# Performance work log

Hardware: AMD Instinct MI355X
Metric: run time of the kernel (lower is better)

## Reference

```python
import jax, jax.numpy as jnp
import numpy as np

NEAR, FAR = 0.0, 6.0
N_COARSE, N_IMP = 128, 64
W = 256


def _sdf_net(p, params):
    w0, b0, w1, b1, w2, b2, w3, b3 = params
    h = jax.nn.softplus(p @ w0 + b0)
    h = jax.nn.softplus(h @ w1 + b1)
    h = jax.nn.softplus(h @ w2 + b2)
    out = h @ w3 + b3  # [..., 1 + W]
    return out[..., 0], out[..., 1:]


def _laplace_cdf(x, beta):
    # CDF of zero-mean Laplace with scale beta (VolSDF density)
    return jnp.where(x <= 0, 0.5 * jnp.exp(x / beta), 1.0 - 0.5 * jnp.exp(-x / beta))


def _sample_pdf(bins, weights, n_samples):
    # bins [R, Nc], weights [R, Nc-1] -> [R, n_samples] (deterministic, perturb=False)
    w = weights + 1e-5
    pdf = w / jnp.sum(w, -1, keepdims=True)
    cdf = jnp.concatenate([jnp.zeros_like(pdf[..., :1]), jnp.cumsum(pdf, -1)], -1)  # [R, Nc]
    u = jnp.linspace(0.0, 1.0, n_samples, dtype=bins.dtype)
    u = jnp.broadcast_to(u, (*bins.shape[:-1], n_samples))
    inds = jax.vmap(jnp.searchsorted)(cdf, u)
    below = jnp.clip(inds - 1, 0, cdf.shape[-1] - 1)
    above = jnp.clip(inds, 0, cdf.shape[-1] - 1)
    cdf_b = jnp.take_along_axis(cdf, below, -1)
    cdf_a = jnp.take_along_axis(cdf, above, -1)
    bin_b = jnp.take_along_axis(bins, below, -1)
    bin_a = jnp.take_along_axis(bins, above, -1)
    denom = jnp.where(cdf_a - cdf_b < 1e-5, 1.0, cdf_a - cdf_b)
    t = (u - cdf_b) / denom
    return bin_b + t * (bin_a - bin_b)


def _transmittance_weights(sigma, deltas):
    a = 1.0 - jnp.exp(-sigma * deltas)
    T = jnp.cumprod(jnp.concatenate([jnp.ones_like(a[..., :1]), 1.0 - a + 1e-10], -1), -1)[..., :-1]
    return a * T


def _render(rays_o, rays_d, alpha, beta, sdf_params, rad_params):
    rays_d = rays_d / jnp.linalg.norm(rays_d, axis=-1, keepdims=True)
    R = rays_o.shape[0]
    a_net = alpha[0]
    b_net = beta[0]
    t = jnp.linspace(0.0, 1.0, N_COARSE, dtype=rays_o.dtype)
    d_coarse = jnp.broadcast_to(NEAR * (1.0 - t) + FAR * t, (R, N_COARSE))

    # --- hierarchical fine sampling (torch.no_grad() in source -> stop_gradient) ---
    pts_c = rays_o[:, None, :] + rays_d[:, None, :] * d_coarse[..., None]
    sdf_c, _ = _sdf_net(pts_c, sdf_params)
    sigma_c = a_net * _laplace_cdf(-sdf_c, b_net)
    deltas_c = jnp.diff(d_coarse, axis=-1)
    w_c = _transmittance_weights(sigma_c[..., :-1], deltas_c)
    d_fine = jax.lax.stop_gradient(_sample_pdf(d_coarse, w_c, N_IMP))

    d_all = jnp.sort(jnp.concatenate([d_coarse, d_fine], -1), -1)  # [R, Nc+Nf]
    pts = rays_o[:, None, :] + rays_d[:, None, :] * d_all[..., None]

    sdf, feat = _sdf_net(pts, sdf_params)
    # analytic surface normals: nabla_p sdf(p)
    grad_fn = jax.grad(lambda p: _sdf_net(p, sdf_params)[0])
    nablas = jax.vmap(grad_fn)(pts.reshape(-1, 3)).reshape(pts.shape)
    normals = nablas / (jnp.linalg.norm(nablas, axis=-1, keepdims=True) + 1e-7)

    vdirs = jnp.broadcast_to(rays_d[:, None, :], pts.shape)
    w0, b0, w1, b1, w2, b2 = rad_params
    h = jnp.concatenate([pts, vdirs, normals, feat], -1)  # [R, Nt, 265]
    h = jax.nn.relu(h @ w0 + b0)
    h = jax.nn.relu(h @ w1 + b1)
    rgb = jax.nn.sigmoid(h @ w2 + b2)  # [R, Nt, 3]

    sigma = a_net * _laplace_cdf(-sdf, b_net)
    deltas = jnp.concatenate([jnp.diff(d_all, axis=-1), jnp.full_like(d_all[..., :1], 1e10)], -1)
    weights = _transmittance_weights(sigma, deltas)  # [R, Nt]
    rgb_map = jnp.sum(weights[..., None] * rgb, axis=-2)  # [R, 3]
    return rgb_map


def setup_inputs() -> dict:
    key = jax.random.key(0)
    ks = jax.random.split(key, 16)
    R = 2048

    def w(k, shape):
        return (jax.random.normal(k, shape, dtype=jnp.float32) / np.sqrt(shape[0])).astype(jnp.float32)

    return {
        'rays_o': jax.random.normal(ks[0], (R, 3), dtype=jnp.float32),
        'rays_d': jax.random.normal(ks[1], (R, 3), dtype=jnp.float32),
        'alpha': jnp.ones((1,), dtype=jnp.float32),
        'beta': jnp.ones((1,), dtype=jnp.float32),
        'sdf_w0': w(ks[2], (3, W)), 'sdf_b0': jnp.zeros((W,), jnp.float32),
        'sdf_w1': w(ks[3], (W, W)), 'sdf_b1': jnp.zeros((W,), jnp.float32),
        'sdf_w2': w(ks[4], (W, W)), 'sdf_b2': jnp.zeros((W,), jnp.float32),
        'sdf_w3': w(ks[5], (W, W + 1)), 'sdf_b3': jnp.zeros((W + 1,), jnp.float32),
        'rad_w0': w(ks[6], (9 + W, W)), 'rad_b0': jnp.zeros((W,), jnp.float32),
        'rad_w1': w(ks[7], (W, W)), 'rad_b1': jnp.zeros((W,), jnp.float32),
        'rad_w2': w(ks[8], (W, 3)), 'rad_b2': jnp.zeros((3,), jnp.float32),
    }


def reference(rays_o, rays_d, alpha, beta,
              sdf_w0, sdf_b0, sdf_w1, sdf_b1, sdf_w2, sdf_b2, sdf_w3, sdf_b3,
              rad_w0, rad_b0, rad_w1, rad_b1, rad_w2, rad_b2):
    sdf_params = (sdf_w0, sdf_b0, sdf_w1, sdf_b1, sdf_w2, sdf_b2, sdf_w3, sdf_b3)
    rad_params = (rad_w0, rad_b0, rad_w1, rad_b1, rad_w2, rad_b2)
    return _render(rays_o, rays_d, alpha, beta, sdf_params, rad_params)
```

## Files before the change

### kernel.cpp

```cpp
#include <hip/hip_runtime.h>
#include <math.h>

#define RAYS 2048

__device__ __forceinline__ float sp_act(float x) {
    return fmaxf(x, 0.0f) + log1pf(expf(-fabsf(x)));
}
__device__ __forceinline__ float lap_cdf(float x, float beta) {
    return (x <= 0.0f) ? 0.5f * expf(x / beta) : 1.0f - 0.5f * expf(-x / beta);
}
__device__ __forceinline__ float sigm(float x) { return 1.0f / (1.0f + expf(-x)); }

template<int MODE, bool BIAS>
__device__ __forceinline__ void tile_mm(const float* __restrict__ Wm,
                                        const float* __restrict__ bias,
                                        const float* IN, float* OUT)
{
    const int t  = threadIdx.x;
    const int j0 = (t & 63) << 2;
    const int p0 = (t >> 6) << 2;
    float acc[4][4];
#pragma unroll
    for (int a = 0; a < 4; ++a)
#pragma unroll
        for (int b = 0; b < 4; ++b) acc[a][b] = 0.0f;

    for (int k = 0; k < 256; k += 4) {
        const float4 w0 = *(const float4*)(Wm + (k + 0) * 256 + j0);
        const float4 w1 = *(const float4*)(Wm + (k + 1) * 256 + j0);
        const float4 w2 = *(const float4*)(Wm + (k + 2) * 256 + j0);
        const float4 w3 = *(const float4*)(Wm + (k + 3) * 256 + j0);
#pragma unroll
        for (int pp = 0; pp < 4; ++pp) {
            const float4 av = *(const float4*)(IN + (p0 + pp) * 256 + k);
            acc[pp][0] = fmaf(av.x, w0.x, acc[pp][0]);
            acc[pp][1] = fmaf(av.x, w0.y, acc[pp][1]);
            acc[pp][2] = fmaf(av.x, w0.z, acc[pp][2]);
            acc[pp][3] = fmaf(av.x, w0.w, acc[pp][3]);
            acc[pp][0] = fmaf(av.y, w1.x, acc[pp][0]);
            acc[pp][1] = fmaf(av.y, w1.y, acc[pp][1]);
            acc[pp][2] = fmaf(av.y, w1.z, acc[pp][2]);
            acc[pp][3] = fmaf(av.y, w1.w, acc[pp][3]);
            acc[pp][0] = fmaf(av.z, w2.x, acc[pp][0]);
            acc[pp][1] = fmaf(av.z, w2.y, acc[pp][1]);
            acc[pp][2] = fmaf(av.z, w2.z, acc[pp][2]);
            acc[pp][3] = fmaf(av.z, w2.w, acc[pp][3]);
            acc[pp][0] = fmaf(av.w, w3.x, acc[pp][0]);
            acc[pp][1] = fmaf(av.w, w3.y, acc[pp][1]);
            acc[pp][2] = fmaf(av.w, w3.z, acc[pp][2]);
            acc[pp][3] = fmaf(av.w, w3.w, acc[pp][3]);
        }
    }
    float bv0 = 0.f, bv1 = 0.f, bv2 = 0.f, bv3 = 0.f;
    if constexpr (BIAS) { bv0 = bias[j0]; bv1 = bias[j0+1]; bv2 = bias[j0+2]; bv3 = bias[j0+3]; }
#pragma unroll
    for (int pp = 0; pp < 4; ++pp) {
        float r0 = acc[pp][0] + bv0;
        float r1 = acc[pp][1] + bv1;
        float r2 = acc[pp][2] + bv2;
        float r3 = acc[pp][3] + bv3;
        if constexpr (MODE == 1) { r0 = sp_act(r0); r1 = sp_act(r1); r2 = sp_act(r2); r3 = sp_act(r3); }
        if constexpr (MODE == 2) { r0 = fmaxf(r0,0.f); r1 = fmaxf(r1,0.f); r2 = fmaxf(r2,0.f); r3 = fmaxf(r3,0.f); }
        *(float4*)(OUT + (p0 + pp) * 256 + j0) = make_float4(r0, r1, r2, r3);
    }
}

__device__ __forceinline__ void rad0_mm(const float* __restrict__ Wm,
                                        const float* __restrict__ bias,
                                        const float (*in9)[12],
                                        const float* F, float* OUT)
{
    const int t  = threadIdx.x;
    const int j0 = (t & 63) << 2;
    const int p0 = (t >> 6) << 2;
    float acc[4][4];
#pragma unroll
    for (int a = 0; a < 4; ++a)
#pragma unroll
        for (int b = 0; b < 4; ++b) acc[a][b] = 0.0f;

#pragma unroll
    for (int k = 0; k < 9; ++k) {
        const float4 w = *(const float4*)(Wm + k * 256 + j0);
#pragma unroll
        for (int pp = 0; pp < 4; ++pp) {
            const float a = in9[p0 + pp][k];
            acc[pp][0] = fmaf(a, w.x, acc[pp][0]);
            acc[pp][1] = fmaf(a, w.y, acc[pp][1]);
            acc[pp][2] = fmaf(a, w.z, acc[pp][2]);
            acc[pp][3] = fmaf(a, w.w, acc[pp][3]);
        }
    }
    for (int k = 0; k < 256; k += 4) {
        const float4 w0 = *(const float4*)(Wm + (9 + k + 0) * 256 + j0);
        const float4 w1 = *(const float4*)(Wm + (9 + k + 1) * 256 + j0);
        const float4 w2 = *(const float4*)(Wm + (9 + k + 2) * 256 + j0);
        const float4 w3 = *(const float4*)(Wm + (9 + k + 3) * 256 + j0);
#pragma unroll
        for (int pp = 0; pp < 4; ++pp) {
            const float4 av = *(const float4*)(F + (p0 + pp) * 256 + k);
            acc[pp][0] = fmaf(av.x, w0.x, acc[pp][0]);
            acc[pp][1] = fmaf(av.x, w0.y, acc[pp][1]);
            acc[pp][2] = fmaf(av.x, w0.z, acc[pp][2]);
            acc[pp][3] = fmaf(av.x, w0.w, acc[pp][3]);
            acc[pp][0] = fmaf(av.y, w1.x, acc[pp][0]);
            acc[pp][1] = fmaf(av.y, w1.y, acc[pp][1]);
            acc[pp][2] = fmaf(av.y, w1.z, acc[pp][2]);
            acc[pp][3] = fmaf(av.y, w1.w, acc[pp][3]);
            acc[pp][0] = fmaf(av.z, w2.x, acc[pp][0]);
            acc[pp][1] = fmaf(av.z, w2.y, acc[pp][1]);
            acc[pp][2] = fmaf(av.z, w2.z, acc[pp][2]);
            acc[pp][3] = fmaf(av.z, w2.w, acc[pp][3]);
            acc[pp][0] = fmaf(av.w, w3.x, acc[pp][0]);
            acc[pp][1] = fmaf(av.w, w3.y, acc[pp][1]);
            acc[pp][2] = fmaf(av.w, w3.z, acc[pp][2]);
            acc[pp][3] = fmaf(av.w, w3.w, acc[pp][3]);
        }
    }
#pragma unroll
    for (int pp = 0; pp < 4; ++pp) {
        float r0 = fmaxf(acc[pp][0] + bias[j0+0], 0.f);
        float r1 = fmaxf(acc[pp][1] + bias[j0+1], 0.f);
        float r2 = fmaxf(acc[pp][2] + bias[j0+2], 0.f);
        float r3 = fmaxf(acc[pp][3] + bias[j0+3], 0.f);
        *(float4*)(OUT + (p0 + pp) * 256 + j0) = make_float4(r0, r1, r2, r3);
    }
}

__global__ __launch_bounds__(256) void prep_kernel(
    const float* __restrict__ w1, const float* __restrict__ w2, const float* __restrict__ w3,
    float* __restrict__ w1T, float* __restrict__ w2T,
    float* __restrict__ w3f, float* __restrict__ w3c0)
{
    const int idx = blockIdx.x * 256 + threadIdx.x;
    const int r = idx >> 8, c = idx & 255;
    w1T[idx] = w1[c * 256 + r];
    w2T[idx] = w2[c * 256 + r];
    w3f[idx] = w3[r * 257 + 1 + c];
    if (idx < 256) w3c0[idx] = w3[idx * 257];
}

__global__ __launch_bounds__(256) void coarse_kernel(
    const float* __restrict__ rays_o, const float* __restrict__ rays_d,
    const float* __restrict__ w0, const float* __restrict__ b0,
    const float* __restrict__ w1, const float* __restrict__ b1,
    const float* __restrict__ w2, const float* __restrict__ b2,
    const float* __restrict__ w3c0, const float* __restrict__ b3,
    float* __restrict__ sdf_out)
{
    __shared__ float A[16 * 256];
    __shared__ float B[16 * 256];
    __shared__ float pts[16][3];
    const int t = threadIdx.x;
    const int base = blockIdx.x * 16;

    if (t < 16) {
        int pg = base + t;
        int ray = pg >> 7, i = pg & 127;
        float ox = rays_o[ray*3+0], oy = rays_o[ray*3+1], oz = rays_o[ray*3+2];
        float dx = rays_d[ray*3+0], dy = rays_d[ray*3+1], dz = rays_d[ray*3+2];
        float n = sqrtf(dx*dx + dy*dy + dz*dz);
        dx /= n; dy /= n; dz /= n;
        float dv = 6.0f * ((float)i / 127.0f);
        pts[t][0] = ox + dx * dv; pts[t][1] = oy + dy * dv; pts[t][2] = oz + dz * dv;
    }
    __syncthreads();
    {
        float wa = w0[t], wb = w0[256 + t], wc = w0[512 + t], bb = b0[t];
#pragma unroll
        for (int p = 0; p < 16; ++p) {
            float z = fmaf(pts[p][0], wa, fmaf(pts[p][1], wb, fmaf(pts[p][2], wc, bb)));
            A[p * 256 + t] = sp_act(z);
        }
    }
    __syncthreads();
    tile_mm<1, true>(w1, b1, A, B); __syncthreads();
    tile_mm<1, true>(w2, b2, B, A); __syncthreads();
    if (t < 16) {
        float s = b3[0];
        for (int k = 0; k < 256; ++k) s = fmaf(A[t * 256 + k], w3c0[k], s);
        sdf_out[base + t] = s;
    }
}

__global__ __launch_bounds__(256) void sample_kernel(
    const float* __restrict__ sdf_c,
    const float* __restrict__ alpha_p, const float* __restrict__ beta_p,
    float* __restrict__ d_all_g)
{
    __shared__ float sig[4][128];
    __shared__ float dc[4][128];
    __shared__ float wbuf[4][127];
    __shared__ float cdf[4][128];
    __shared__ float dfine[4][64];
    __shared__ float dall[4][192];
    const int t = threadIdx.x;
    const int wv = t >> 6, lane = t & 63;
    const int ray = blockIdx.x * 4 + wv;
    const float alpha = alpha_p[0], beta = beta_p[0];

    for (int i = lane; i < 128; i += 64) {
        float s = sdf_c[ray * 128 + i];
        sig[wv][i] = alpha * lap_cdf(-s, beta);
        dc[wv][i] = 6.0f * ((float)i / 127.0f);
    }
    __syncthreads();
    if (lane == 0) {
        float T = 1.0f, S = 0.0f;
        for (int i = 0; i < 127; ++i) {
            float delta = dc[wv][i + 1] - dc[wv][i];
            float a = 1.0f - expf(-sig[wv][i] * delta);
            float w = a * T;
            T *= (1.0f - a + 1e-10f);
            wbuf[wv][i] = w;
            S += (w + 1e-5f);
        }
        float c = 0.0f;
        cdf[wv][0] = 0.0f;
        for (int i = 0; i < 127; ++i) {
            c += (wbuf[wv][i] + 1e-5f) / S;
            cdf[wv][i + 1] = c;
        }
    }
    __syncthreads();
    {
        float u = (float)lane / 63.0f;
        int lo = 0, hi = 128;
        while (lo < hi) { int m = (lo + hi) >> 1; if (cdf[wv][m] < u) lo = m + 1; else hi = m; }
        int below = lo - 1; if (below < 0) below = 0; if (below > 127) below = 127;
        int above = lo; if (above > 127) above = 127;
        float cb = cdf[wv][below], ca = cdf[wv][above];
        float bb = dc[wv][below], ba = dc[wv][above];
        float den = ca - cb; if (den < 1e-5f) den = 1.0f;
        float tt = (u - cb) / den;
        dfine[wv][lane] = bb + tt * (ba - bb);
    }
    __syncthreads();
    {
        float v = dfine[wv][lane];
        int lo = 0, hi = 128;
        while (lo < hi) { int m = (lo + hi) >> 1; if (dc[wv][m] <= v) lo = m + 1; else hi = m; }
        dall[wv][lane + lo] = v;
    }
    for (int i = lane; i < 128; i += 64) {
        float v = dc[wv][i];
        int lo = 0, hi = 64;
        while (lo < hi) { int m = (lo + hi) >> 1; if (dfine[wv][m] < v) lo = m + 1; else hi = m; }
        dall[wv][i + lo] = v;
    }
    __syncthreads();
    for (int i = lane; i < 192; i += 64) d_all_g[ray * 192 + i] = dall[wv][i];
}

__global__ __launch_bounds__(256) void fine_kernel(
    const float* __restrict__ rays_o, const float* __restrict__ rays_d,
    const float* __restrict__ dall_g,
    const float* __restrict__ w0, const float* __restrict__ b0,
    const float* __restrict__ w1, const float* __restrict__ b1,
    const float* __restrict__ w2, const float* __restrict__ b2,
    const float* __restrict__ w3f, const float* __restrict__ w3c0,
    const float* __restrict__ b3,
    const float* __restrict__ w1T, const float* __restrict__ w2T,
    const float* __restrict__ rw0, const float* __restrict__ rb0,
    const float* __restrict__ rw1, const float* __restrict__ rb1,
    const float* __restrict__ rw2, const float* __restrict__ rb2,
    float* __restrict__ fsdf, float* __restrict__ frgb)
{
    __shared__ float X[16 * 256];
    __shared__ float Y[16 * 256];
    __shared__ float Z[16 * 256];
    __shared__ float F[16 * 256];
    __shared__ float in9[16][12];
    const int t = threadIdx.x;
    const int base = blockIdx.x * 16;

    if (t < 16) {
        int pg = base + t;
        int ray = pg / 192, i = pg - ray * 192;
        float ox = rays_o[ray*3+0], oy = rays_o[ray*3+1], oz = rays_o[ray*3+2];
        float dx = rays_d[ray*3+0], dy = rays_d[ray*3+1], dz = rays_d[ray*3+2];
        float n = sqrtf(dx*dx + dy*dy + dz*dz);
        dx /= n; dy /= n; dz /= n;
        float dv = dall_g[ray * 192 + i];
        in9[t][0] = ox + dx * dv; in9[t][1] = oy + dy * dv; in9[t][2] = oz + dz * dv;
        in9[t][3] = dx; in9[t][4] = dy; in9[t][5] = dz;
    }
    __syncthreads();
    {
        float wa = w0[t], wb = w0[256 + t], wc = w0[512 + t], bb = b0[t];
#pragma unroll
        for (int p = 0; p < 16; ++p) {
            float z = fmaf(in9[p][0], wa, fmaf(in9[p][1], wb, fmaf(in9[p][2], wc, bb)));
            X[p * 256 + t] = sp_act(z);
        }
    }
    __syncthreads();
    tile_mm<1, true>(w1, b1, X, Y); __syncthreads();
    tile_mm<1, true>(w2, b2, Y, X); __syncthreads();
    tile_mm<0, true>(w3f, b3 + 1, X, F); __syncthreads();
    if (t < 16) {
        float s = b3[0];
        for (int k = 0; k < 256; ++k) s = fmaf(X[t * 256 + k], w3c0[k], s);
        fsdf[base + t] = s;
    }
    __syncthreads();
    {
        float wc0 = w3c0[t];
#pragma unroll
        for (int p = 0; p < 16; ++p) {
            float h = X[p * 256 + t];
            X[p * 256 + t] = (1.0f - expf(-h)) * wc0;
        }
    }
    __syncthreads();
    tile_mm<0, false>(w2T, nullptr, X, Z); __syncthreads();
    {
#pragma unroll
        for (int p = 0; p < 16; ++p) {
            float h = Y[p * 256 + t];
            Z[p * 256 + t] *= (1.0f - expf(-h));
        }
    }
    __syncthreads();
    tile_mm<0, false>(w1T, nullptr, Z, X); __syncthreads();
    {
        float wa = w0[t], wb = w0[256 + t], wc = w0[512 + t], bb = b0[t];
#pragma unroll
        for (int p = 0; p < 16; ++p) {
            float z = fmaf(in9[p][0], wa, fmaf(in9[p][1], wb, fmaf(in9[p][2], wc, bb)));
            X[p * 256 + t] *= sigm(z);
        }
    }
    __syncthreads();
    if (t < 48) {
        int p = t / 3, c = t - p * 3;
        float s = 0.0f;
        for (int k = 0; k < 256; ++k) s = fmaf(w0[c * 256 + k], X[p * 256 + k], s);
        in9[p][6 + c] = s;
    }
    __syncthreads();
    if (t < 16) {
        float nx = in9[t][6], ny = in9[t][7], nz = in9[t][8];
        float inv = 1.0f / (sqrtf(nx*nx + ny*ny + nz*nz) + 1e-7f);
        in9[t][6] = nx * inv; in9[t][7] = ny * inv; in9[t][8] = nz * inv;
    }
    __syncthreads();
    rad0_mm(rw0, rb0, in9, F, Y); __syncthreads();
    tile_mm<2, true>(rw1, rb1, Y, X); __syncthreads();
    if (t < 48) {
        int p = t / 3, c = t - p * 3;
        float s = rb2[c];
        for (int k = 0; k < 256; ++k) s = fmaf(X[p * 256 + k], rw2[k * 3 + c], s);
        frgb[(base + p) * 3 + c] = sigm(s);
    }
}

__global__ __launch_bounds__(256) void composite_kernel(
    const float* __restrict__ dall_g, const float* __restrict__ fsdf,
    const float* __restrict__ frgb,
    const float* __restrict__ alpha_p, const float* __restrict__ beta_p,
    float* __restrict__ out)
{
    __shared__ float aa[4][192];
    __shared__ float da[4][192];
    const int t = threadIdx.x;
    const int wv = t >> 6, lane = t & 63;
    const int ray = blockIdx.x * 4 + wv;
    const float alpha = alpha_p[0], beta = beta_p[0];

    for (int i = lane; i < 192; i += 64) da[wv][i] = dall_g[ray * 192 + i];
    __syncthreads();
    for (int i = lane; i < 192; i += 64) {
        float s = fsdf[ray * 192 + i];
        float sg = alpha * lap_cdf(-s, beta);
        float delta = (i < 191) ? (da[wv][i + 1] - da[wv][i]) : 1e10f;
        aa[wv][i] = 1.0f - expf(-sg * delta);
    }
    __syncthreads();
    if (lane == 0) {
        float T = 1.0f, r0 = 0.f, r1 = 0.f, r2 = 0.f;
        for (int i = 0; i < 192; ++i) {
            float a = aa[wv][i];
            float w = a * T;
            T *= (1.0f - a + 1e-10f);
            const float* rp = frgb + (ray * 192 + i) * 3;
            r0 = fmaf(w, rp[0], r0);
            r1 = fmaf(w, rp[1], r1);
            r2 = fmaf(w, rp[2], r2);
        }
        out[ray * 3 + 0] = r0; out[ray * 3 + 1] = r1; out[ray * 3 + 2] = r2;
    }
}

extern "C" void kernel_launch(void* const* d_in, const int* in_sizes, int n_in,
                              void* d_out, int out_size, void* d_ws, size_t ws_size,
                              hipStream_t stream) {
    const float* rays_o = (const float*)d_in[0];
    const float* rays_d = (const float*)d_in[1];
    const float* alpha  = (const float*)d_in[2];
    const float* beta   = (const float*)d_in[3];
    const float* sw0 = (const float*)d_in[4];
    const float* sb0 = (const float*)d_in[5];
    const float* sw1 = (const float*)d_in[6];
    const float* sb1 = (const float*)d_in[7];
    const float* sw2 = (const float*)d_in[8];
    const float* sb2 = (const float*)d_in[9];
    const float* sw3 = (const float*)d_in[10];
    const float* sb3 = (const float*)d_in[11];
    const float* rw0 = (const float*)d_in[12];
    const float* rb0 = (const float*)d_in[13];
    const float* rw1 = (const float*)d_in[14];
    const float* rb1 = (const float*)d_in[15];
    const float* rw2 = (const float*)d_in[16];
    const float* rb2 = (const float*)d_in[17];

    float* ws = (float*)d_ws;
    float* w1T   = ws;  ws += 65536;
    float* w2T   = ws;  ws += 65536;
    float* w3f   = ws;  ws += 65536;
    float* w3c0  = ws;  ws += 256;
    float* sdf_c = ws;  ws += RAYS * 128;
    float* dall  = ws;  ws += RAYS * 192;
    float* fsdf  = ws;  ws += RAYS * 192;
    float* frgb  = ws;  ws += RAYS * 192 * 3;

    prep_kernel<<<256, 256, 0, stream>>>(sw1, sw2, sw3, w1T, w2T, w3f, w3c0);
    coarse_kernel<<<RAYS * 128 / 16, 256, 0, stream>>>(
        rays_o, rays_d, sw0, sb0, sw1, sb1, sw2, sb2, w3c0, sb3, sdf_c);
    sample_kernel<<<RAYS / 4, 256, 0, stream>>>(sdf_c, alpha, beta, dall);
    fine_kernel<<<RAYS * 192 / 16, 256, 0, stream>>>(
        rays_o, rays_d, dall,
        sw0, sb0, sw1, sb1, sw2, sb2, w3f, w3c0, sb3,
        w1T, w2T, rw0, rb0, rw1, rb1, rw2, rb2,
        fsdf, frgb);
    composite_kernel<<<RAYS / 4, 256, 0, stream>>>(dall, fsdf, frgb, alpha, beta, (float*)d_out);
}
```

Before: 7.496 ms.

## Replace scalar FP32 MLP GEMMs with split-bf16 MFMA matrix-core GEMMs

```diff
diff --git a/kernel.cpp b/kernel.cpp
--- a/kernel.cpp
+++ b/kernel.cpp
@@ -3,6 +3,10 @@
 
 #define RAYS 2048
 
+typedef unsigned short ushort_t;
+typedef short bf16x8 __attribute__((ext_vector_type(8)));
+typedef float f32x4 __attribute__((ext_vector_type(4)));
+
 __device__ __forceinline__ float sp_act(float x) {
     return fmaxf(x, 0.0f) + log1pf(expf(-fabsf(x)));
 }
@@ -11,174 +15,180 @@
 }
 __device__ __forceinline__ float sigm(float x) { return 1.0f / (1.0f + expf(-x)); }
 
-template<int MODE, bool BIAS>
-__device__ __forceinline__ void tile_mm(const float* __restrict__ Wm,
-                                        const float* __restrict__ bias,
-                                        const float* IN, float* OUT)
+__device__ __forceinline__ ushort_t f2bf(float x) {
+    union { float f; unsigned int u; } c; c.f = x;
+    unsigned int u = c.u + 0x7FFF + ((c.u >> 16) & 1);
+    return (ushort_t)(u >> 16);
+}
+__device__ __forceinline__ float bf2f(ushort_t s) {
+    union { unsigned int u; float f; } c; c.u = ((unsigned int)s) << 16;
+    return c.f;
+}
+__device__ __forceinline__ void split2(float v, ushort_t& hi, ushort_t& lo) {
+    hi = f2bf(v);
+    lo = f2bf(v - bf2f(hi));
+}
+template<int P>
+__device__ __forceinline__ int aidx(int p, int n) { return ((n >> 3) * P + p) * 16 + (n & 7); }
+
+__device__ __forceinline__ void mfma16x16x32(f32x4& c, bf16x8 a, bf16x8 b) {
+    asm("v_mfma_f32_16x16x32_bf16 %0, %1, %2, %0" : "+v"(c) : "v"(a), "v"(b));
+}
+
+template<int MODE, int KSTEPS, bool BIAS, int PM, bool SPLIT>
+__device__ __forceinline__ void mfma_gemm(const ushort_t* __restrict__ A,
+                                          const ushort_t* __restrict__ Bp,
+                                          const float* __restrict__ bias,
+                                          ushort_t* __restrict__ OUT)
 {
-    const int t  = threadIdx.x;
-    const int j0 = (t & 63) << 2;
-    const int p0 = (t >> 6) << 2;
-    float acc[4][4];
-#pragma unroll
-    for (int a = 0; a < 4; ++a)
-#pragma unroll
-        for (int b = 0; b < 4; ++b) acc[a][b] = 0.0f;
-
-    for (int k = 0; k < 256; k += 4) {
-        const float4 w0 = *(const float4*)(Wm + (k + 0) * 256 + j0);
-        const float4 w1 = *(const float4*)(Wm + (k + 1) * 256 + j0);
-        const float4 w2 = *(const float4*)(Wm + (k + 2) * 256 + j0);
-        const float4 w3 = *(const float4*)(Wm + (k + 3) * 256 + j0);
-#pragma unroll
-        for (int pp = 0; pp < 4; ++pp) {
-            const float4 av = *(const float4*)(IN + (p0 + pp) * 256 + k);
-            acc[pp][0] = fmaf(av.x, w0.x, acc[pp][0]);
-            acc[pp][1] = fmaf(av.x, w0.y, acc[pp][1]);
-            acc[pp][2] = fmaf(av.x, w0.z, acc[pp][2]);
-            acc[pp][3] = fmaf(av.x, w0.w, acc[pp][3]);
-            acc[pp][0] = fmaf(av.y, w1.x, acc[pp][0]);
-            acc[pp][1] = fmaf(av.y, w1.y, acc[pp][1]);
-            acc[pp][2] = fmaf(av.y, w1.z, acc[pp][2]);
-            acc[pp][3] = fmaf(av.y, w1.w, acc[pp][3]);
-            acc[pp][0] = fmaf(av.z, w2.x, acc[pp][0]);
-            acc[pp][1] = fmaf(av.z, w2.y, acc[pp][1]);
-            acc[pp][2] = fmaf(av.z, w2.z, acc[pp][2]);
-            acc[pp][3] = fmaf(av.z, w2.w, acc[pp][3]);
-            acc[pp][0] = fmaf(av.w, w3.x, acc[pp][0]);
-            acc[pp][1] = fmaf(av.w, w3.y, acc[pp][1]);
-            acc[pp][2] = fmaf(av.w, w3.z, acc[pp][2]);
-            acc[pp][3] = fmaf(av.w, w3.w, acc[pp][3]);
-        }
-    }
-    float bv0 = 0.f, bv1 = 0.f, bv2 = 0.f, bv3 = 0.f;
-    if constexpr (BIAS) { bv0 = bias[j0]; bv1 = bias[j0+1]; bv2 = bias[j0+2]; bv3 = bias[j0+3]; }
-#pragma unroll
-    for (int pp = 0; pp < 4; ++pp) {
-        float r0 = acc[pp][0] + bv0;
-        float r1 = acc[pp][1] + bv1;
-        float r2 = acc[pp][2] + bv2;
-        float r3 = acc[pp][3] + bv3;
-        if constexpr (MODE == 1) { r0 = sp_act(r0); r1 = sp_act(r1); r2 = sp_act(r2); r3 = sp_act(r3); }
-        if constexpr (MODE == 2) { r0 = fmaxf(r0,0.f); r1 = fmaxf(r1,0.f); r2 = fmaxf(r2,0.f); r3 = fmaxf(r3,0.f); }
-        *(float4*)(OUT + (p0 + pp) * 256 + j0) = make_float4(r0, r1, r2, r3);
-    }
-}
-
-__device__ __forceinline__ void rad0_mm(const float* __restrict__ Wm,
-                                        const float* __restrict__ bias,
-                                        const float (*in9)[12],
-                                        const float* F, float* OUT)
-{
-    const int t  = threadIdx.x;
-    const int j0 = (t & 63) << 2;
-    const int p0 = (t >> 6) << 2;
-    float acc[4][4];
-#pragma unroll
-    for (int a = 0; a < 4; ++a)
-#pragma unroll
-        for (int b = 0; b < 4; ++b) acc[a][b] = 0.0f;
-
-#pragma unroll
-    for (int k = 0; k < 9; ++k) {
-        const float4 w = *(const float4*)(Wm + k * 256 + j0);
-#pragma unroll
-        for (int pp = 0; pp < 4; ++pp) {
-            const float a = in9[p0 + pp][k];
-            acc[pp][0] = fmaf(a, w.x, acc[pp][0]);
-            acc[pp][1] = fmaf(a, w.y, acc[pp][1]);
-            acc[pp][2] = fmaf(a, w.z, acc[pp][2]);
-            acc[pp][3] = fmaf(a, w.w, acc[pp][3]);
-        }
-    }
-    for (int k = 0; k < 256; k += 4) {
-        const float4 w0 = *(const float4*)(Wm + (9 + k + 0) * 256 + j0);
-        const float4 w1 = *(const float4*)(Wm + (9 + k + 1) * 256 + j0);
-        const float4 w2 = *(const float4*)(Wm + (9 + k + 2) * 256 + j0);
-        const float4 w3 = *(const float4*)(Wm + (9 + k + 3) * 256 + j0);
-#pragma unroll
-        for (int pp = 0; pp < 4; ++pp) {
-            const float4 av = *(const float4*)(F + (p0 + pp) * 256 + k);
-            acc[pp][0] = fmaf(av.x, w0.x, acc[pp][0]);
-            acc[pp][1] = fmaf(av.x, w0.y, acc[pp][1]);
-            acc[pp][2] = fmaf(av.x, w0.z, acc[pp][2]);
-            acc[pp][3] = fmaf(av.x, w0.w, acc[pp][3]);
-            acc[pp][0] = fmaf(av.y, w1.x, acc[pp][0]);
-            acc[pp][1] = fmaf(av.y, w1.y, acc[pp][1]);
-            acc[pp][2] = fmaf(av.y, w1.z, acc[pp][2]);
-            acc[pp][3] = fmaf(av.y, w1.w, acc[pp][3]);
-            acc[pp][0] = fmaf(av.z, w2.x, acc[pp][0]);
-            acc[pp][1] = fmaf(av.z, w2.y, acc[pp][1]);
-            acc[pp][2] = fmaf(av.z, w2.z, acc[pp][2]);
-            acc[pp][3] = fmaf(av.z, w2.w, acc[pp][3]);
-            acc[pp][0] = fmaf(av.w, w3.x, acc[pp][0]);
-            acc[pp][1] = fmaf(av.w, w3.y, acc[pp][1]);
-            acc[pp][2] = fmaf(av.w, w3.z, acc[pp][2]);
-            acc[pp][3] = fmaf(av.w, w3.w, acc[pp][3]);
-        }
-    }
-#pragma unroll
-    for (int pp = 0; pp < 4; ++pp) {
-        float r0 = fmaxf(acc[pp][0] + bias[j0+0], 0.f);
-        float r1 = fmaxf(acc[pp][1] + bias[j0+1], 0.f);
-        float r2 = fmaxf(acc[pp][2] + bias[j0+2], 0.f);
-        float r3 = fmaxf(acc[pp][3] + bias[j0+3], 0.f);
-        *(float4*)(OUT + (p0 + pp) * 256 + j0) = make_float4(r0, r1, r2, r3);
+    constexpr int P = PM * 16;
+    const int t = threadIdx.x;
+    const int wave = t >> 6, lane = t & 63;
+    const int r16 = lane & 15, kg = lane >> 4;
+    f32x4 acc[PM][4];
+#pragma unroll
+    for (int m = 0; m < PM; ++m)
+#pragma unroll
+        for (int nf = 0; nf < 4; ++nf) acc[m][nf] = 0.0f;
+
+#pragma unroll
+    for (int ks = 0; ks < KSTEPS; ++ks) {
+        bf16x8 ah[PM], al[PM], bh[4], bl[4];
+#pragma unroll
+        for (int m = 0; m < PM; ++m) {
+            const int ab = ((ks * 4 + kg) * P + m * 16 + r16) * 16;
+            ah[m] = *(const bf16x8*)(A + ab);
+            if (SPLIT) al[m] = *(const bf16x8*)(A + ab + 8);
+        }
+#pragma unroll
+        for (int nf = 0; nf < 4; ++nf) {
+            const int n = wave * 64 + nf * 16 + r16;
+            if (SPLIT) {
+                const int bb = ((ks * 256 + n) * 4 + kg) * 16;
+                bh[nf] = *(const bf16x8*)(Bp + bb);
+                bl[nf] = *(const bf16x8*)(Bp + bb + 8);
+            } else {
+                const int bb = ((ks * 256 + n) * 4 + kg) * 8;
+                bh[nf] = *(const bf16x8*)(Bp + bb);
+            }
+        }
+#pragma unroll
+        for (int m = 0; m < PM; ++m)
+#pragma unroll
+            for (int nf = 0; nf < 4; ++nf) {
+                mfma16x16x32(acc[m][nf], ah[m], bh[nf]);
+                if (SPLIT) {
+                    mfma16x16x32(acc[m][nf], ah[m], bl[nf]);
+                    mfma16x16x32(acc[m][nf], al[m], bh[nf]);
+                }
+            }
+    }
+#pragma unroll
+    for (int nf = 0; nf < 4; ++nf) {
+        const int n = wave * 64 + nf * 16 + r16;
+        float bv = 0.0f;
+        if (BIAS) bv = bias[n];
+#pragma unroll
+        for (int m = 0; m < PM; ++m) {
+#pragma unroll
+            for (int r = 0; r < 4; ++r) {
+                const int p = m * 16 + kg * 4 + r;
+                float v = acc[m][nf][r] + bv;
+                if (MODE == 1) v = sp_act(v);
+                if (MODE == 2) v = fmaxf(v, 0.0f);
+                ushort_t hi, lo;
+                split2(v, hi, lo);
+                const int ob = aidx<P>(p, n);
+                OUT[ob] = hi; OUT[ob + 8] = lo;
+            }
+        }
     }
 }
 
 __global__ __launch_bounds__(256) void prep_kernel(
     const float* __restrict__ w1, const float* __restrict__ w2, const float* __restrict__ w3,
-    float* __restrict__ w1T, float* __restrict__ w2T,
-    float* __restrict__ w3f, float* __restrict__ w3c0)
+    const float* __restrict__ rw0, const float* __restrict__ rw1,
+    ushort_t* __restrict__ pw1T, ushort_t* __restrict__ pw2T, ushort_t* __restrict__ pw3T,
+    ushort_t* __restrict__ pw2B, ushort_t* __restrict__ pw1B,
+    ushort_t* __restrict__ pwR1, ushort_t* __restrict__ pwR0,
+    float* __restrict__ w3c0)
 {
-    const int idx = blockIdx.x * 256 + threadIdx.x;
-    const int r = idx >> 8, c = idx & 255;
-    w1T[idx] = w1[c * 256 + r];
-    w2T[idx] = w2[c * 256 + r];
-    w3f[idx] = w3[r * 257 + 1 + c];
-    if (idx < 256) w3c0[idx] = w3[idx * 257];
-}
-
-__global__ __launch_bounds__(256) void coarse_kernel(
+    const int k = blockIdx.x, mat = blockIdx.y, n = threadIdx.x;
+    const int K = (mat == 6) ? 288 : 256;
+    if (k >= K) return;
+    float v = 0.0f; ushort_t* dst = pw1T; bool lite = false;
+    switch (mat) {
+        case 0: v = w1[k * 256 + n]; dst = pw1T; break;
+        case 1: v = w2[k * 256 + n]; dst = pw2T; break;
+        case 2: v = w3[k * 257 + 1 + n]; dst = pw3T;
+                if (n == 0) w3c0[k] = w3[k * 257];
+                break;
+        case 3: v = w2[n * 256 + k]; dst = pw2B; lite = true; break;
+        case 4: v = w1[n * 256 + k]; dst = pw1B; lite = true; break;
+        case 5: v = rw1[k * 256 + n]; dst = pwR1; break;
+        case 6: v = (k < 256) ? rw0[(9 + k) * 256 + n]
+                  : (k < 265 ? rw0[(k - 256) * 256 + n] : 0.0f);
+                dst = pwR0; break;
+    }
+    if (lite) {
+        dst[(((k >> 5) * 256 + n) * 4 + ((k >> 3) & 3)) * 8 + (k & 7)] = f2bf(v);
+    } else {
+        const int b = (((k >> 5) * 256 + n) * 4 + ((k >> 3) & 3)) * 16 + (k & 7);
+        ushort_t hi, lo; split2(v, hi, lo);
+        dst[b] = hi; dst[b + 8] = lo;
+    }
+}
+
+__global__ __launch_bounds__(256, 1) void coarse_kernel(
     const float* __restrict__ rays_o, const float* __restrict__ rays_d,
     const float* __restrict__ w0, const float* __restrict__ b0,
-    const float* __restrict__ w1, const float* __restrict__ b1,
-    const float* __restrict__ w2, const float* __restrict__ b2,
+    const float* __restrict__ b1, const float* __restrict__ b2,
+    const ushort_t* __restrict__ pw1T, const ushort_t* __restrict__ pw2T,
     const float* __restrict__ w3c0, const float* __restrict__ b3,
     float* __restrict__ sdf_out)
 {
-    __shared__ float A[16 * 256];
-    __shared__ float B[16 * 256];
-    __shared__ float pts[16][3];
+    __shared__ ushort_t bufA[32768], bufB[32768];
+    __shared__ float geo[64][3];
+    __shared__ float red[256];
     const int t = threadIdx.x;
-    const int base = blockIdx.x * 16;
-
-    if (t < 16) {
-        int pg = base + t;
-        int ray = pg >> 7, i = pg & 127;
+    const int base = blockIdx.x * 64;
+
+    if (t < 64) {
+        const int p = t, pg = base + p;
+        const int ray = pg >> 7, i = pg & 127;
         float ox = rays_o[ray*3+0], oy = rays_o[ray*3+1], oz = rays_o[ray*3+2];
         float dx = rays_d[ray*3+0], dy = rays_d[ray*3+1], dz = rays_d[ray*3+2];
-        float n = sqrtf(dx*dx + dy*dy + dz*dz);
-        dx /= n; dy /= n; dz /= n;
+        float nm = sqrtf(dx*dx + dy*dy + dz*dz);
+        dx /= nm; dy /= nm; dz /= nm;
         float dv = 6.0f * ((float)i / 127.0f);
-        pts[t][0] = ox + dx * dv; pts[t][1] = oy + dy * dv; pts[t][2] = oz + dz * dv;
-    }
-    __syncthreads();
-    {
-        float wa = w0[t], wb = w0[256 + t], wc = w0[512 + t], bb = b0[t];
-#pragma unroll
-        for (int p = 0; p < 16; ++p) {
-            float z = fmaf(pts[p][0], wa, fmaf(pts[p][1], wb, fmaf(pts[p][2], wc, bb)));
-            A[p * 256 + t] = sp_act(z);
-        }
-    }
-    __syncthreads();
-    tile_mm<1, true>(w1, b1, A, B); __syncthreads();
-    tile_mm<1, true>(w2, b2, B, A); __syncthreads();
-    if (t < 16) {
-        float s = b3[0];
-        for (int k = 0; k < 256; ++k) s = fmaf(A[t * 256 + k], w3c0[k], s);
+        geo[p][0] = ox + dx * dv; geo[p][1] = oy + dy * dv; geo[p][2] = oz + dz * dv;
+    }
+    __syncthreads();
+    {
+        const int n = t;
+        float wa = w0[n], wb = w0[256 + n], wc = w0[512 + n], bb = b0[n];
+        for (int p = 0; p < 64; ++p) {
+            float z = fmaf(geo[p][0], wa, fmaf(geo[p][1], wb, fmaf(geo[p][2], wc, bb)));
+            ushort_t hi, lo; split2(sp_act(z), hi, lo);
+            const int ob = aidx<64>(p, n);
+            bufA[ob] = hi; bufA[ob + 8] = lo;
+        }
+    }
+    __syncthreads();
+    mfma_gemm<1, 8, true, 4, true>(bufA, pw1T, b1, bufB); __syncthreads();
+    mfma_gemm<1, 8, true, 4, true>(bufB, pw2T, b2, bufA); __syncthreads();
+    {
+        const int p = t >> 2, nb = t & 3;
+        float s = 0.0f;
+        for (int k = nb * 64; k < nb * 64 + 64; ++k) {
+            const int ob = aidx<64>(p, k);
+            s = fmaf(bf2f(bufA[ob]) + bf2f(bufA[ob + 8]), w3c0[k], s);
+        }
+        red[t] = s;
+    }
+    __syncthreads();
+    if (t < 64) {
+        float s = b3[0] + red[t*4] + red[t*4+1] + red[t*4+2] + red[t*4+3];
         sdf_out[base + t] = s;
     }
 }
@@ -252,106 +262,160 @@
     for (int i = lane; i < 192; i += 64) d_all_g[ray * 192 + i] = dall[wv][i];
 }
 
-__global__ __launch_bounds__(256) void fine_kernel(
+__global__ __launch_bounds__(256, 1) void fine_kernel(
     const float* __restrict__ rays_o, const float* __restrict__ rays_d,
     const float* __restrict__ dall_g,
     const float* __restrict__ w0, const float* __restrict__ b0,
-    const float* __restrict__ w1, const float* __restrict__ b1,
-    const float* __restrict__ w2, const float* __restrict__ b2,
-    const float* __restrict__ w3f, const float* __restrict__ w3c0,
-    const float* __restrict__ b3,
-    const float* __restrict__ w1T, const float* __restrict__ w2T,
-    const float* __restrict__ rw0, const float* __restrict__ rb0,
-    const float* __restrict__ rw1, const float* __restrict__ rb1,
+    const float* __restrict__ b1, const float* __restrict__ b2, const float* __restrict__ b3,
+    const ushort_t* __restrict__ pw1T, const ushort_t* __restrict__ pw2T,
+    const ushort_t* __restrict__ pw3T, const ushort_t* __restrict__ pw2B,
+    const ushort_t* __restrict__ pw1B,
+    const ushort_t* __restrict__ pwR0, const ushort_t* __restrict__ pwR1,
+    const float* __restrict__ w3c0,
+    const float* __restrict__ rb0, const float* __restrict__ rb1,
     const float* __restrict__ rw2, const float* __restrict__ rb2,
     float* __restrict__ fsdf, float* __restrict__ frgb)
 {
-    __shared__ float X[16 * 256];
-    __shared__ float Y[16 * 256];
-    __shared__ float Z[16 * 256];
-    __shared__ float F[16 * 256];
-    __shared__ float in9[16][12];
+    __shared__ ushort_t buf0[16384], buf1[16384], buf2[16384];
+    __shared__ ushort_t fbuf[18432];
+    __shared__ float geo[32][6];
+    __shared__ float red[768];
     const int t = threadIdx.x;
-    const int base = blockIdx.x * 16;
-
-    if (t < 16) {
-        int pg = base + t;
-        int ray = pg / 192, i = pg - ray * 192;
+    const int base = blockIdx.x * 32;
+
+    if (t < 32) {
+        const int p = t, pg = base + p;
+        const int ray = pg / 192, i = pg - ray * 192;
         float ox = rays_o[ray*3+0], oy = rays_o[ray*3+1], oz = rays_o[ray*3+2];
         float dx = rays_d[ray*3+0], dy = rays_d[ray*3+1], dz = rays_d[ray*3+2];
-        float n = sqrtf(dx*dx + dy*dy + dz*dz);
-        dx /= n; dy /= n; dz /= n;
+        float nm = sqrtf(dx*dx + dy*dy + dz*dz);
+        dx /= nm; dy /= nm; dz /= nm;
         float dv = dall_g[ray * 192 + i];
-        in9[t][0] = ox + dx * dv; in9[t][1] = oy + dy * dv; in9[t][2] = oz + dz * dv;
-        in9[t][3] = dx; in9[t][4] = dy; in9[t][5] = dz;
-    }
-    __syncthreads();
-    {
-        float wa = w0[t], wb = w0[256 + t], wc = w0[512 + t], bb = b0[t];
-#pragma unroll
-        for (int p = 0; p < 16; ++p) {
-            float z = fmaf(in9[p][0], wa, fmaf(in9[p][1], wb, fmaf(in9[p][2], wc, bb)));
-            X[p * 256 + t] = sp_act(z);
-        }
-    }
-    __syncthreads();
-    tile_mm<1, true>(w1, b1, X, Y); __syncthreads();
-    tile_mm<1, true>(w2, b2, Y, X); __syncthreads();
-    tile_mm<0, true>(w3f, b3 + 1, X, F); __syncthreads();
-    if (t < 16) {
+        float px = ox + dx * dv, py = oy + dy * dv, pz = oz + dz * dv;
+        geo[p][0] = px; geo[p][1] = py; geo[p][2] = pz;
+        geo[p][3] = dx; geo[p][4] = dy; geo[p][5] = dz;
+        ushort_t hi, lo; int ob;
+        split2(px, hi, lo); ob = aidx<32>(p, 256); fbuf[ob] = hi; fbuf[ob+8] = lo;
+        split2(py, hi, lo); ob = aidx<32>(p, 257); fbuf[ob] = hi; fbuf[ob+8] = lo;
+        split2(pz, hi, lo); ob = aidx<32>(p, 258); fbuf[ob] = hi; fbuf[ob+8] = lo;
+        split2(dx, hi, lo); ob = aidx<32>(p, 259); fbuf[ob] = hi; fbuf[ob+8] = lo;
+        split2(dy, hi, lo); ob = aidx<32>(p, 260); fbuf[ob] = hi; fbuf[ob+8] = lo;
+        split2(dz, hi, lo); ob = aidx<32>(p, 261); fbuf[ob] = hi; fbuf[ob+8] = lo;
+    }
+    for (int idx = t; idx < 32 * 23; idx += 256) {
+        int p = idx & 31, k = 265 + (idx >> 5);
+        const int ob = aidx<32>(p, k);
+        fbuf[ob] = 0; fbuf[ob + 8] = 0;
+    }
+    __syncthreads();
+    {
+        const int n = t;
+        float wa = w0[n], wb = w0[256 + n], wc = w0[512 + n], bb = b0[n];
+        for (int p = 0; p < 32; ++p) {
+            float z = fmaf(geo[p][0], wa, fmaf(geo[p][1], wb, fmaf(geo[p][2], wc, bb)));
+            ushort_t hi, lo; split2(sp_act(z), hi, lo);
+            const int ob = aidx<32>(p, n);
+            buf0[ob] = hi; buf0[ob + 8] = lo;
+        }
+    }
+    __syncthreads();
+    mfma_gemm<1, 8, true, 2, true>(buf0, pw1T, b1, buf1); __syncthreads();
+    mfma_gemm<1, 8, true, 2, true>(buf1, pw2T, b2, buf2); __syncthreads();
+    mfma_gemm<0, 8, true, 2, true>(buf2, pw3T, b3 + 1, fbuf); __syncthreads();
+    {
+        const int p = t >> 3, nb = t & 7;
+        float s = 0.0f;
+        for (int k = nb * 32; k < nb * 32 + 32; ++k) {
+            const int ob = aidx<32>(p, k);
+            s = fmaf(bf2f(buf2[ob]) + bf2f(buf2[ob + 8]), w3c0[k], s);
+        }
+        red[t] = s;
+        const int n = t;
+        const float wc0 = w3c0[n];
+        for (int p2 = 0; p2 < 32; ++p2) {
+            const int ob = aidx<32>(p2, n);
+            float h = bf2f(buf2[ob]) + bf2f(buf2[ob + 8]);
+            ushort_t hi, lo; split2((1.0f - expf(-h)) * wc0, hi, lo);
+            buf0[ob] = hi; buf0[ob + 8] = lo;
+        }
+    }
+    __syncthreads();
+    if (t < 32) {
         float s = b3[0];
-        for (int k = 0; k < 256; ++k) s = fmaf(X[t * 256 + k], w3c0[k], s);
+#pragma unroll
+        for (int nb = 0; nb < 8; ++nb) s += red[t * 8 + nb];
         fsdf[base + t] = s;
     }
     __syncthreads();
-    {
-        float wc0 = w3c0[t];
-#pragma unroll
-        for (int p = 0; p < 16; ++p) {
-            float h = X[p * 256 + t];
-            X[p * 256 + t] = (1.0f - expf(-h)) * wc0;
-        }
-    }
-    __syncthreads();
-    tile_mm<0, false>(w2T, nullptr, X, Z); __syncthreads();
-    {
-#pragma unroll
-        for (int p = 0; p < 16; ++p) {
-            float h = Y[p * 256 + t];
-            Z[p * 256 + t] *= (1.0f - expf(-h));
-        }
-    }
-    __syncthreads();
-    tile_mm<0, false>(w1T, nullptr, Z, X); __syncthreads();
-    {
-        float wa = w0[t], wb = w0[256 + t], wc = w0[512 + t], bb = b0[t];
-#pragma unroll
-        for (int p = 0; p < 16; ++p) {
-            float z = fmaf(in9[p][0], wa, fmaf(in9[p][1], wb, fmaf(in9[p][2], wc, bb)));
-            X[p * 256 + t] *= sigm(z);
-        }
-    }
-    __syncthreads();
-    if (t < 48) {
-        int p = t / 3, c = t - p * 3;
-        float s = 0.0f;
-        for (int k = 0; k < 256; ++k) s = fmaf(w0[c * 256 + k], X[p * 256 + k], s);
-        in9[p][6 + c] = s;
-    }
-    __syncthreads();
-    if (t < 16) {
-        float nx = in9[t][6], ny = in9[t][7], nz = in9[t][8];
+    mfma_gemm<0, 8, false, 2, false>(buf0, pw2B, nullptr, buf2); __syncthreads();
+    {
+        const int n = t;
+        for (int p = 0; p < 32; ++p) {
+            const int ob = aidx<32>(p, n);
+            float g = bf2f(buf2[ob]) + bf2f(buf2[ob + 8]);
+            float h = bf2f(buf1[ob]) + bf2f(buf1[ob + 8]);
+            ushort_t hi, lo; split2(g * (1.0f - expf(-h)), hi, lo);
+            buf2[ob] = hi; buf2[ob + 8] = lo;
+        }
+    }
+    __syncthreads();
+    mfma_gemm<0, 8, false, 2, false>(buf2, pw1B, nullptr, buf0); __syncthreads();
+    {
+        const int p = t >> 3, nb = t & 7;
+        float px = geo[p][0], py = geo[p][1], pz = geo[p][2];
+        float pa = 0.f, pb = 0.f, pc = 0.f;
+        for (int k = nb * 32; k < nb * 32 + 32; ++k) {
+            float wa = w0[k], wb = w0[256+k], wc = w0[512+k];
+            float z = fmaf(px, wa, fmaf(py, wb, fmaf(pz, wc, b0[k])));
+            float g = bf2f(buf0[aidx<32>(p, k)]) * sigm(z);
+            pa = fmaf(wa, g, pa); pb = fmaf(wb, g, pb); pc = fmaf(wc, g, pc);
+        }
+        red[t * 3 + 0] = pa; red[t * 3 + 1] = pb; red[t * 3 + 2] = pc;
+    }
+    __syncthreads();
+    if (t < 32) {
+        const int p = t;
+        float nx = 0.f, ny = 0.f, nz = 0.f;
+#pragma unroll
+        for (int nb = 0; nb < 8; ++nb) {
+            nx += red[(p * 8 + nb) * 3 + 0];
+            ny += red[(p * 8 + nb) * 3 + 1];
+            nz += red[(p * 8 + nb) * 3 + 2];
+        }
         float inv = 1.0f / (sqrtf(nx*nx + ny*ny + nz*nz) + 1e-7f);
-        in9[t][6] = nx * inv; in9[t][7] = ny * inv; in9[t][8] = nz * inv;
-    }
-    __syncthreads();
-    rad0_mm(rw0, rb0, in9, F, Y); __syncthreads();
-    tile_mm<2, true>(rw1, rb1, Y, X); __syncthreads();
-    if (t < 48) {
-        int p = t / 3, c = t - p * 3;
-        float s = rb2[c];
-        for (int k = 0; k < 256; ++k) s = fmaf(X[p * 256 + k], rw2[k * 3 + c], s);
-        frgb[(base + p) * 3 + c] = sigm(s);
+        ushort_t hi, lo; int ob;
+        split2(nx * inv, hi, lo); ob = aidx<32>(p, 262); fbuf[ob] = hi; fbuf[ob+8] = lo;
+        split2(ny * inv, hi, lo); ob = aidx<32>(p, 263); fbuf[ob] = hi; fbuf[ob+8] = lo;
+        split2(nz * inv, hi, lo); ob = aidx<32>(p, 264); fbuf[ob] = hi; fbuf[ob+8] = lo;
+    }
+    __syncthreads();
+    mfma_gemm<2, 9, true, 2, true>(fbuf, pwR0, rb0, buf1); __syncthreads();
+    mfma_gemm<2, 8, true, 2, true>(buf1, pwR1, rb1, buf2); __syncthreads();
+    {
+        const int p = t >> 3, nb = t & 7;
+        float s0 = 0.f, s1 = 0.f, s2 = 0.f;
+        for (int k = nb * 32; k < nb * 32 + 32; ++k) {
+            const int ob = aidx<32>(p, k);
+            float f = bf2f(buf2[ob]) + bf2f(buf2[ob + 8]);
+            s0 = fmaf(f, rw2[k*3+0], s0);
+            s1 = fmaf(f, rw2[k*3+1], s1);
+            s2 = fmaf(f, rw2[k*3+2], s2);
+        }
+        red[t * 3 + 0] = s0; red[t * 3 + 1] = s1; red[t * 3 + 2] = s2;
+    }
+    __syncthreads();
+    if (t < 32) {
+        const int p = t;
+        float s0 = rb2[0], s1 = rb2[1], s2 = rb2[2];
+#pragma unroll
+        for (int nb = 0; nb < 8; ++nb) {
+            s0 += red[(p * 8 + nb) * 3 + 0];
+            s1 += red[(p * 8 + nb) * 3 + 1];
+            s2 += red[(p * 8 + nb) * 3 + 2];
+        }
+        frgb[(base + p) * 3 + 0] = sigm(s0);
+        frgb[(base + p) * 3 + 1] = sigm(s1);
+        frgb[(base + p) * 3 + 2] = sigm(s2);
     }
 }
 
@@ -414,24 +478,31 @@
     const float* rw2 = (const float*)d_in[16];
     const float* rb2 = (const float*)d_in[17];
 
-    float* ws = (float*)d_ws;
-    float* w1T   = ws;  ws += 65536;
-    float* w2T   = ws;  ws += 65536;
-    float* w3f   = ws;  ws += 65536;
-    float* w3c0  = ws;  ws += 256;
-    float* sdf_c = ws;  ws += RAYS * 128;
-    float* dall  = ws;  ws += RAYS * 192;
-    float* fsdf  = ws;  ws += RAYS * 192;
-    float* frgb  = ws;  ws += RAYS * 192 * 3;
-
-    prep_kernel<<<256, 256, 0, stream>>>(sw1, sw2, sw3, w1T, w2T, w3f, w3c0);
-    coarse_kernel<<<RAYS * 128 / 16, 256, 0, stream>>>(
-        rays_o, rays_d, sw0, sb0, sw1, sb1, sw2, sb2, w3c0, sb3, sdf_c);
+    ushort_t* wsu = (ushort_t*)d_ws;
+    ushort_t* pw1T = wsu;
+    ushort_t* pw2T = pw1T + 131072;
+    ushort_t* pw3T = pw2T + 131072;
+    ushort_t* pwR1 = pw3T + 131072;
+    ushort_t* pwR0 = pwR1 + 131072;
+    ushort_t* pw2B = pwR0 + 147456;
+    ushort_t* pw1B = pw2B + 65536;
+    float* wsf = (float*)(pw1B + 65536);
+    float* w3c0  = wsf;               wsf += 256;
+    float* sdf_c = wsf;               wsf += RAYS * 128;
+    float* dall  = wsf;               wsf += RAYS * 192;
+    float* fsdf  = wsf;               wsf += RAYS * 192;
+    float* frgb  = wsf;               wsf += RAYS * 192 * 3;
+
+    prep_kernel<<<dim3(288, 7), 256, 0, stream>>>(
+        sw1, sw2, sw3, rw0, rw1, pw1T, pw2T, pw3T, pw2B, pw1B, pwR1, pwR0, w3c0);
+    coarse_kernel<<<RAYS * 128 / 64, 256, 0, stream>>>(
+        rays_o, rays_d, sw0, sb0, sb1, sb2, pw1T, pw2T, w3c0, sb3, sdf_c);
     sample_kernel<<<RAYS / 4, 256, 0, stream>>>(sdf_c, alpha, beta, dall);
-    fine_kernel<<<RAYS * 192 / 16, 256, 0, stream>>>(
+    fine_kernel<<<RAYS * 192 / 32, 256, 0, stream>>>(
         rays_o, rays_d, dall,
-        sw0, sb0, sw1, sb1, sw2, sb2, w3f, w3c0, sb3,
-        w1T, w2T, rw0, rb0, rw1, rb1, rw2, rb2,
+        sw0, sb0, sb1, sb2, sb3,
+        pw1T, pw2T, pw3T, pw2B, pw1B, pwR0, pwR1,
+        w3c0, rb0, rb1, rw2, rb2,
         fsdf, frgb);
     composite_kernel<<<RAYS / 4, 256, 0, stream>>>(dall, fsdf, frgb, alpha, beta, (float*)d_out);
 }
```

New measurement: 6.583 ms. 12.2% less time.
